# Kernel tuning notes

Measured on AMD Instinct MI355X. Metric: run time of the kernel, lower is better.

Reference implementation:

```python
import jax, jax.numpy as jnp
import numpy as np

D_MODEL = 1024
NUM_SLOTS = 4096
MIN_K = 8
MAX_K = 32


def setup_inputs() -> dict:
    key = jax.random.key(0)
    k1, k2, k3 = jax.random.split(key, 3)
    x = jax.random.normal(k1, (4, 1024, D_MODEL), dtype=jnp.float32)
    param_pool = 0.02 * jax.random.normal(k2, (NUM_SLOTS, D_MODEL), dtype=jnp.float32)
    w_router = 0.02 * jax.random.normal(k3, (D_MODEL, NUM_SLOTS), dtype=jnp.float32)
    return {"x": x, "param_pool": param_pool, "w_router": w_router}


def _route(x, w_router):
    # Router: linear projection to slot logits, softmax, dynamic top-k in [MIN_K, MAX_K].
    logits = jnp.einsum('bsd,dn->bsn', x, w_router)           # [B,S,N]
    probs = jax.nn.softmax(logits, axis=-1)
    top_probs, indices = jax.lax.top_k(probs, MAX_K)          # [B,S,K]
    # dynamic k: always keep first MIN_K slots; keep up to MAX_K while prob > uniform
    pos = jnp.arange(MAX_K)
    keep = (pos < MIN_K) | (top_probs > (1.0 / NUM_SLOTS))    # [B,S,K] bool
    keep_f = keep.astype(top_probs.dtype)
    masked = top_probs * keep_f
    weights = masked / (jnp.sum(masked, axis=-1, keepdims=True) + 1e-9)
    # load-balancing aux loss: N * sum(mean_prob_per_slot * frac_tokens_routed_per_slot)
    mean_probs = jnp.mean(probs, axis=(0, 1))                 # [N]
    counts = jnp.zeros((NUM_SLOTS,), dtype=jnp.float32).at[indices.reshape(-1)].add(keep_f.reshape(-1))
    frac = counts / (jnp.sum(keep_f) + 1e-9)
    aux_loss = NUM_SLOTS * jnp.sum(mean_probs * frac)
    return indices, weights, keep, aux_loss


def reference(x, param_pool, w_router):
    indices, weights, keep, aux_loss = _route(x, w_router)
    selected_params = param_pool[indices]                      # [B,S,K,D] gather
    proj = jnp.einsum('bsd,bskd->bsk', x, selected_params)     # per-token dot scores
    weighted_proj = proj * weights
    output = jnp.einsum('bsk,bskd->bsd', weighted_proj, selected_params)
    flat_indices = indices.reshape(-1)
    flat_keep = keep.reshape(-1)
    touched = jnp.zeros((NUM_SLOTS,), dtype=jnp.bool_).at[flat_indices].max(flat_keep)
    active_count = jnp.sum(touched)
    return (output, aux_loss, active_count)
```

## Files before the change

### kernel.cpp

```cpp
#include <hip/hip_runtime.h>
#include <math.h>
#include <stdint.h>

#define D_MODEL   1024
#define NUM_SLOTS 4096
#define N_TOKENS  4096
#define MIN_K     8
#define MAX_K     32
#define KP        1024
#define NSTEP     32

typedef _Float16 f16x8 __attribute__((ext_vector_type(8)));
typedef _Float16 f16x4 __attribute__((ext_vector_type(4)));
typedef float    f32x4 __attribute__((ext_vector_type(4)));

__device__ __forceinline__ void gload16(const void* g, void* l) {
    __builtin_amdgcn_global_load_lds((const __attribute__((address_space(1))) void*)g,
                                     (__attribute__((address_space(3))) void*)l,
                                     16, 0, 0);
}

__device__ __forceinline__ uint32_t bf16rn(float f) {
    uint32_t u = __float_as_uint(f);
    return (u + 0x7FFFu + ((u >> 16) & 1u)) >> 16;
}

__device__ __forceinline__ uint32_t ford(float f) {
    uint32_t b = __float_as_uint(f);
    return b ^ (uint32_t)(((int32_t)b >> 31) | 0x80000000);
}

__global__ __launch_bounds__(256) void pack_all(const float* __restrict__ x,
                                                const float* __restrict__ w,
                                                const float* __restrict__ pool,
                                                _Float16* __restrict__ A,
                                                _Float16* __restrict__ BT,
                                                uint32_t* __restrict__ poolbf,
                                                float* __restrict__ clr) {
    __shared__ float tile[64][65];
    const int bid = blockIdx.x;
    const int tid = threadIdx.x;

    if (bid < 4096) {
        if (bid < 32) clr[bid * 256 + tid] = 0.f;
        const int i = bid * 256 + tid;
        const float4 v = reinterpret_cast<const float4*>(x)[i];
        const int t = i >> 8;
        const int d = (i & 255) << 2;
        f16x4 hi;
        hi[0] = (_Float16)v.x; hi[1] = (_Float16)v.y;
        hi[2] = (_Float16)v.z; hi[3] = (_Float16)v.w;
        *(f16x4*)(A + (size_t)t * KP + d) = hi;
    } else if (bid < 5120) {
        const int b2 = bid - 4096;
        const int n0 = (b2 & 63) * 64;
        const int k0 = (b2 >> 6) * 64;
        {
            const int c  = tid & 63;
            const int r0 = tid >> 6;
#pragma unroll
            for (int i = 0; i < 16; ++i) {
                const int r = r0 * 16 + i;
                tile[r][c] = w[(size_t)(k0 + r) * NUM_SLOTS + n0 + c];
            }
        }
        __syncthreads();
        const int nl  = tid >> 2;
        const int kl0 = (tid & 3) * 16;
        _Float16* rowp = BT + (size_t)(n0 + nl) * KP + k0;
#pragma unroll
        for (int j4 = 0; j4 < 16; j4 += 4) {
            f16x4 hi;
#pragma unroll
            for (int u = 0; u < 4; ++u)
                hi[u] = (_Float16)tile[kl0 + j4 + u][nl];
            *(f16x4*)(rowp + kl0 + j4) = hi;
        }
    } else {
        const size_t i = (size_t)(bid - 5120) * 256 + tid;
        const float4* s4 = reinterpret_cast<const float4*>(pool);
        const float4 a = s4[2 * i];
        const float4 b = s4[2 * i + 1];
        uint4 u;
        u.x = bf16rn(a.x) | (bf16rn(a.y) << 16);
        u.y = bf16rn(a.z) | (bf16rn(a.w) << 16);
        u.z = bf16rn(b.x) | (bf16rn(b.y) << 16);
        u.w = bf16rn(b.z) | (bf16rn(b.w) << 16);
        reinterpret_cast<uint4*>(poolbf)[i] = u;
    }
}

#define STAGE_A(NXT, S2) \
    gload16(gA0 + (size_t)(S2) * 32, (void*)(AsF + (NXT) * 8192 + tid * 8)); \
    gload16(gA1 + (size_t)(S2) * 32, (void*)(AsF + (NXT) * 8192 + 4096 + tid * 8));
#define STAGE_B(NXT, S2) \
    gload16(gB0 + (size_t)(S2) * 32, (void*)(BsF + (NXT) * 8192 + tid * 8)); \
    gload16(gB1 + (size_t)(S2) * 32, (void*)(BsF + (NXT) * 8192 + 4096 + tid * 8));

#define MM(AF, M) \
    acc[M][0] = __builtin_amdgcn_mfma_f32_16x16x32_f16(AF, bf0, acc[M][0], 0, 0, 0); \
    acc[M][1] = __builtin_amdgcn_mfma_f32_16x16x32_f16(AF, bf1, acc[M][1], 0, 0, 0); \
    acc[M][2] = __builtin_amdgcn_mfma_f32_16x16x32_f16(AF, bf2, acc[M][2], 0, 0, 0); \
    acc[M][3] = __builtin_amdgcn_mfma_f32_16x16x32_f16(AF, bf3, acc[M][3], 0, 0, 0);

#define GSTEP(S, CUR, NXT) do { \
    const _Float16* a_ = AsF + (CUR) * 8192; \
    const _Float16* b_ = BsF + (CUR) * 8192; \
    f16x8 bf0 = *(const f16x8*)(b_ + offB0); \
    f16x8 bf1 = *(const f16x8*)(b_ + offB1); \
    f16x8 bf2 = *(const f16x8*)(b_ + offB2); \
    f16x8 bf3 = *(const f16x8*)(b_ + offB3); \
    f16x8 a0 = *(const f16x8*)(a_ + offA0); \
    f16x8 a1 = *(const f16x8*)(a_ + offA1); \
    f16x8 a2 = *(const f16x8*)(a_ + offA2); \
    f16x8 a3 = *(const f16x8*)(a_ + offA3); \
    if ((S) + 2 < NSTEP) { STAGE_A(NXT, (S) + 2) } \
    asm volatile("" ::: "memory"); \
    __builtin_amdgcn_s_barrier(); \
    __builtin_amdgcn_s_setprio(1); \
    MM(a0, 0) MM(a1, 1) MM(a2, 2) MM(a3, 3) \
    __builtin_amdgcn_s_setprio(0); \
    asm volatile("" ::: "memory"); \
    __builtin_amdgcn_s_barrier(); \
    a0 = *(const f16x8*)(a_ + offA4); \
    a1 = *(const f16x8*)(a_ + offA5); \
    a2 = *(const f16x8*)(a_ + offA6); \
    a3 = *(const f16x8*)(a_ + offA7); \
    if ((S) + 2 < NSTEP) { STAGE_B(NXT, (S) + 2) } \
    asm volatile("" ::: "memory"); \
    __builtin_amdgcn_s_barrier(); \
    __builtin_amdgcn_s_setprio(1); \
    MM(a0, 4) MM(a1, 5) MM(a2, 6) MM(a3, 7) \
    __builtin_amdgcn_s_setprio(0); \
    if ((S) < NSTEP - 2) { asm volatile("s_waitcnt vmcnt(4)" ::: "memory"); } \
    else                 { asm volatile("s_waitcnt vmcnt(0)" ::: "memory"); } \
    __builtin_amdgcn_s_barrier(); \
} while (0)

__global__ __launch_bounds__(512, 2) void gemm256(const _Float16* __restrict__ A,
                                                  const _Float16* __restrict__ BT,
                                                  float* __restrict__ C,
                                                  int nbm) {
    __shared__ _Float16 AsF[4 * 8192];
    __shared__ _Float16 BsF[4 * 8192];
    const int tid  = threadIdx.x;
    const int lane = tid & 63;
    const int wv   = tid >> 6;
    const int wm   = wv >> 2;
    const int wn   = wv & 3;

    int brow, bcol;
    {
        const int bid = blockIdx.x;
        if (nbm == 16) {
            const int xcd = bid & 7;
            const int l   = bid >> 3;
            brow = (xcd & 3) * 4 + (l & 3);
            bcol = (xcd >> 2) * 8 + (l >> 2);
        } else {
            brow = bid >> 4;
            bcol = bid & 15;
        }
    }
    const size_t bm = (size_t)brow * 256;
    const size_t bn = (size_t)bcol * 256;

    const int rowA = tid >> 2;
    const int slot = tid & 3;
    const int sswz = slot ^ ((rowA >> 1) & 3);
    const _Float16* gA0 = A  + (bm + rowA) * (size_t)KP + sswz * 8;
    const _Float16* gA1 = A  + (bm + rowA + 128) * (size_t)KP + sswz * 8;
    const _Float16* gB0 = BT + (bn + rowA) * (size_t)KP + sswz * 8;
    const _Float16* gB1 = BT + (bn + rowA + 128) * (size_t)KP + sswz * 8;

    int offA0, offA1, offA2, offA3, offA4, offA5, offA6, offA7;
    int offB0, offB1, offB2, offB3;
    {
        const int r15 = lane & 15, ls = lane >> 4;
#define AOFF(M) (((wm) * 128 + (M) * 16 + r15) * 32 + \
                 ((ls ^ ((((wm) * 128 + (M) * 16 + r15) >> 1) & 3)) * 8))
#define BOFF(N) (((wn) * 64 + (N) * 16 + r15) * 32 + \
                 ((ls ^ ((((wn) * 64 + (N) * 16 + r15) >> 1) & 3)) * 8))
        offA0 = AOFF(0); offA1 = AOFF(1); offA2 = AOFF(2); offA3 = AOFF(3);
        offA4 = AOFF(4); offA5 = AOFF(5); offA6 = AOFF(6); offA7 = AOFF(7);
        offB0 = BOFF(0); offB1 = BOFF(1); offB2 = BOFF(2); offB3 = BOFF(3);
#undef AOFF
#undef BOFF
    }

    f32x4 acc[8][4] = {};

    STAGE_A(0, 0) STAGE_B(0, 0)
    STAGE_A(1, 1) STAGE_B(1, 1)
    asm volatile("s_waitcnt vmcnt(4)" ::: "memory");
    __builtin_amdgcn_s_barrier();

    for (int s4 = 0; s4 < NSTEP; s4 += 4) {
        GSTEP(s4 + 0, 0, 2);
        GSTEP(s4 + 1, 1, 3);
        GSTEP(s4 + 2, 2, 0);
        GSTEP(s4 + 3, 3, 1);
    }

    const size_t crow = bm + wm * 128 + ((lane >> 4) << 2);
    const size_t ccol = bn + wn * 64 + (lane & 15);
#pragma unroll
    for (int m = 0; m < 8; ++m)
#pragma unroll
        for (int r = 0; r < 4; ++r) {
            float* cp = C + (crow + m * 16 + r) * (size_t)NUM_SLOTS + ccol;
#pragma unroll
            for (int n = 0; n < 4; ++n) cp[n * 16] = acc[m][n][r];
        }
}

#define RECOMP(G, A, B, Cc, D) do { \
    uint32_t t0 = (msk & (1u << (A)))  ? k##A  : 0u; \
    uint32_t t1 = (msk & (1u << (B)))  ? k##B  : 0u; \
    uint32_t t2 = (msk & (1u << (Cc))) ? k##Cc : 0u; \
    uint32_t t3 = (msk & (1u << (D)))  ? k##D  : 0u; \
    t0 = t0 > t1 ? t0 : t1; t2 = t2 > t3 ? t2 : t3; \
    gm##G = t0 > t2 ? t0 : t2; } while (0)

#define UNPK8(q, a0,a1,a2,a3,a4,a5,a6,a7) \
    a0 = __uint_as_float((q).x << 16); a1 = __uint_as_float((q).x & 0xFFFF0000u); \
    a2 = __uint_as_float((q).y << 16); a3 = __uint_as_float((q).y & 0xFFFF0000u); \
    a4 = __uint_as_float((q).z << 16); a5 = __uint_as_float((q).z & 0xFFFF0000u); \
    a6 = __uint_as_float((q).w << 16); a7 = __uint_as_float((q).w & 0xFFFF0000u);

__global__ __launch_bounds__(256) void router_kernel(
    const float* __restrict__ logits,
    const float* __restrict__ x,
    const uint32_t* __restrict__ poolbf,
    float* __restrict__ out,
    float2* __restrict__ minv,
    float* __restrict__ counts) {
    __shared__ float    s_union[NUM_SLOTS];
    __shared__ uint32_t s_cand[128];
    __shared__ float    s_redv[4];

    const int tid  = threadIdx.x;
    const int w    = tid >> 6;
    const int lane = tid & 63;
    const int wseg = w << 10;
    const int t    = blockIdx.x;

    const float4* lrow4 =
        reinterpret_cast<const float4*>(logits + (size_t)t * NUM_SLOTS + wseg);

    float4 lv0, lv1, lv2, lv3;
    lv0 = lrow4[lane];
    lv1 = lrow4[lane + 64];
    lv2 = lrow4[lane + 128];
    lv3 = lrow4[lane + 192];
    reinterpret_cast<float4*>(s_union + wseg)[lane]       = lv0;
    reinterpret_cast<float4*>(s_union + wseg)[lane + 64]  = lv1;
    reinterpret_cast<float4*>(s_union + wseg)[lane + 128] = lv2;
    reinterpret_cast<float4*>(s_union + wseg)[lane + 192] = lv3;
    float lmax = fmaxf(fmaxf(fmaxf(lv0.x, lv0.y), fmaxf(lv0.z, lv0.w)),
                       fmaxf(fmaxf(lv1.x, lv1.y), fmaxf(lv1.z, lv1.w)));
    lmax = fmaxf(lmax, fmaxf(fmaxf(lv2.x, lv2.y), fmaxf(lv2.z, lv2.w)));
    lmax = fmaxf(lmax, fmaxf(fmaxf(lv3.x, lv3.y), fmaxf(lv3.z, lv3.w)));
#pragma unroll
    for (int o = 32; o; o >>= 1) lmax = fmaxf(lmax, __shfl_xor(lmax, o));
    if (lane == 0) s_redv[w] = lmax;
    __syncthreads();
    const float m = fmaxf(fmaxf(s_redv[0], s_redv[1]), fmaxf(s_redv[2], s_redv[3]));
    __syncthreads();

    float lsum;
    {
        float4 ev0, ev1, ev2, ev3;
        ev0.x = __expf(lv0.x - m); ev0.y = __expf(lv0.y - m);
        ev0.z = __expf(lv0.z - m); ev0.w = __expf(lv0.w - m);
        ev1.x = __expf(lv1.x - m); ev1.y = __expf(lv1.y - m);
        ev1.z = __expf(lv1.z - m); ev1.w = __expf(lv1.w - m);
        ev2.x = __expf(lv2.x - m); ev2.y = __expf(lv2.y - m);
        ev2.z = __expf(lv2.z - m); ev2.w = __expf(lv2.w - m);
        ev3.x = __expf(lv3.x - m); ev3.y = __expf(lv3.y - m);
        ev3.z = __expf(lv3.z - m); ev3.w = __expf(lv3.w - m);
        lsum = (ev0.x + ev0.y + ev0.z + ev0.w) + (ev1.x + ev1.y + ev1.z + ev1.w) +
               (ev2.x + ev2.y + ev2.z + ev2.w) + (ev3.x + ev3.y + ev3.z + ev3.w);
    }
#pragma unroll
    for (int o = 32; o; o >>= 1) lsum += __shfl_xor(lsum, o);
    if (lane == 0) s_redv[w] = lsum;
    __syncthreads();
    const float inv = 1.0f / (s_redv[0] + s_redv[1] + s_redv[2] + s_redv[3]);
    if (tid == 0) minv[t] = make_float2(m, inv);

    const int kb = wseg + 4 * lane;
    uint32_t k0  = (ford(lv0.x) & 0xFFFFF000u) | (uint32_t)(4095 - (kb + 0));
    uint32_t k1  = (ford(lv0.y) & 0xFFFFF000u) | (uint32_t)(4095 - (kb + 1));
    uint32_t k2  = (ford(lv0.z) & 0xFFFFF000u) | (uint32_t)(4095 - (kb + 2));
    uint32_t k3  = (ford(lv0.w) & 0xFFFFF000u) | (uint32_t)(4095 - (kb + 3));
    uint32_t k4  = (ford(lv1.x) & 0xFFFFF000u) | (uint32_t)(4095 - (kb + 256));
    uint32_t k5  = (ford(lv1.y) & 0xFFFFF000u) | (uint32_t)(4095 - (kb + 257));
    uint32_t k6  = (ford(lv1.z) & 0xFFFFF000u) | (uint32_t)(4095 - (kb + 258));
    uint32_t k7  = (ford(lv1.w) & 0xFFFFF000u) | (uint32_t)(4095 - (kb + 259));
    uint32_t k8  = (ford(lv2.x) & 0xFFFFF000u) | (uint32_t)(4095 - (kb + 512));
    uint32_t k9  = (ford(lv2.y) & 0xFFFFF000u) | (uint32_t)(4095 - (kb + 513));
    uint32_t k10 = (ford(lv2.z) & 0xFFFFF000u) | (uint32_t)(4095 - (kb + 514));
    uint32_t k11 = (ford(lv2.w) & 0xFFFFF000u) | (uint32_t)(4095 - (kb + 515));
    uint32_t k12 = (ford(lv3.x) & 0xFFFFF000u) | (uint32_t)(4095 - (kb + 768));
    uint32_t k13 = (ford(lv3.y) & 0xFFFFF000u) | (uint32_t)(4095 - (kb + 769));
    uint32_t k14 = (ford(lv3.z) & 0xFFFFF000u) | (uint32_t)(4095 - (kb + 770));
    uint32_t k15 = (ford(lv3.w) & 0xFFFFF000u) | (uint32_t)(4095 - (kb + 771));

    uint32_t msk = 0xFFFFu;
    uint32_t gm0, gm1, gm2, gm3;
    RECOMP(0, 0, 1, 2, 3); RECOMP(1, 4, 5, 6, 7);
    RECOMP(2, 8, 9, 10, 11); RECOMP(3, 12, 13, 14, 15);

    uint32_t kept = 0;
    for (int it = 0; it < 32; ++it) {
        uint32_t best = gm0;
        if (gm1 > best) best = gm1;
        if (gm2 > best) best = gm2;
        if (gm3 > best) best = gm3;
        uint32_t wb = best;
#pragma unroll
        for (int o = 32; o; o >>= 1) {
            const uint32_t p = __shfl_xor(wb, o);
            if (p > wb) wb = p;
        }
        if (lane == it) kept = wb;
        if (best == wb) {
            const int idx = 4095 - (int)(wb & 0xFFFu);
            const int rem = idx - kb;
            const int jj = rem >> 8;
            msk &= ~(1u << (4 * jj + (rem & 3)));
            switch (jj) {
                case 0:  RECOMP(0, 0, 1, 2, 3); break;
                case 1:  RECOMP(1, 4, 5, 6, 7); break;
                case 2:  RECOMP(2, 8, 9, 10, 11); break;
                default: RECOMP(3, 12, 13, 14, 15); break;
            }
        }
    }
    if (lane < 32) s_cand[w * 32 + lane] = kept;
    __syncthreads();

    uint32_t v0 = s_cand[lane];
    uint32_t v1 = s_cand[64 + lane];
#pragma unroll
    for (int k = 2; k <= 128; k <<= 1) {
#pragma unroll
        for (int j = k >> 1; j > 0; j >>= 1) {
            if (j == 64) {
                const uint32_t a = v0 > v1 ? v0 : v1;
                const uint32_t b = v0 > v1 ? v1 : v0;
                v0 = a; v1 = b;
            } else {
                const bool jl = (lane & j) == 0;
                {
                    const uint32_t p = __shfl_xor(v0, j);
                    const bool km = ((lane & k) == 0) == jl;
                    v0 = ((p > v0) == km) ? p : v0;
                }
                {
                    const uint32_t p = __shfl_xor(v1, j);
                    const bool km = (((lane + 64) & k) == 0) == jl;
                    v1 = ((p > v1) == km) ? p : v1;
                }
            }
        }
    }

    const int slotv = 4095 - (int)(v0 & 0xFFFu);
    float pv = 0.f;
    if (lane < 32) pv = __expf(s_union[slotv] - m) * inv;
    const bool kp = (lane < MIN_K) || (pv > (1.0f / 4096.0f));
    float wsum = kp ? pv : 0.f;
#pragma unroll
    for (int o = 32; o; o >>= 1) wsum += __shfl_xor(wsum, o);
    const float wgtl = kp ? pv / (wsum + 1e-9f) : 0.f;
    if (w == 0 && lane < 32 && kp) atomicAdd(&counts[slotv], 1.0f);
    __syncthreads();

    const float4* x4 = reinterpret_cast<const float4*>(x + (size_t)t * D_MODEL);
    const float4 xa0 = x4[2 * lane];
    const float4 xb0 = x4[2 * lane + 1];
    const float4 xa1 = x4[2 * lane + 128];
    const float4 xb1 = x4[2 * lane + 129];
    float4 oa0 = {0,0,0,0}, ob0 = {0,0,0,0}, oa1 = {0,0,0,0}, ob1 = {0,0,0,0};

#pragma unroll
    for (int ii = 0; ii < 8; ++ii) {
        const int   i     = w * 8 + ii;
        const int   slotg = __shfl(slotv, i);
        const float wgt   = __shfl(wgtl, i);
        if (wgt != 0.f) {
            const uint4* pr = reinterpret_cast<const uint4*>(poolbf + (size_t)slotg * (D_MODEL / 2));
            const uint4 q0 = pr[lane];
            const uint4 q1 = pr[lane + 64];
            float pA0,pA1,pA2,pA3,pA4,pA5,pA6,pA7;
            float pB0,pB1,pB2,pB3,pB4,pB5,pB6,pB7;
            UNPK8(q0, pA0,pA1,pA2,pA3,pA4,pA5,pA6,pA7)
            UNPK8(q1, pB0,pB1,pB2,pB3,pB4,pB5,pB6,pB7)
            float d;
            d = xa0.x * pA0;
            d = fmaf(xa0.y, pA1, d); d = fmaf(xa0.z, pA2, d); d = fmaf(xa0.w, pA3, d);
            d = fmaf(xb0.x, pA4, d); d = fmaf(xb0.y, pA5, d); d = fmaf(xb0.z, pA6, d); d = fmaf(xb0.w, pA7, d);
            d = fmaf(xa1.x, pB0, d); d = fmaf(xa1.y, pB1, d); d = fmaf(xa1.z, pB2, d); d = fmaf(xa1.w, pB3, d);
            d = fmaf(xb1.x, pB4, d); d = fmaf(xb1.y, pB5, d); d = fmaf(xb1.z, pB6, d); d = fmaf(xb1.w, pB7, d);
#pragma unroll
            for (int o = 32; o; o >>= 1) d += __shfl_xor(d, o);
            const float wp = d * wgt;
            oa0.x = fmaf(wp, pA0, oa0.x); oa0.y = fmaf(wp, pA1, oa0.y);
            oa0.z = fmaf(wp, pA2, oa0.z); oa0.w = fmaf(wp, pA3, oa0.w);
            ob0.x = fmaf(wp, pA4, ob0.x); ob0.y = fmaf(wp, pA5, ob0.y);
            ob0.z = fmaf(wp, pA6, ob0.z); ob0.w = fmaf(wp, pA7, ob0.w);
            oa1.x = fmaf(wp, pB0, oa1.x); oa1.y = fmaf(wp, pB1, oa1.y);
            oa1.z = fmaf(wp, pB2, oa1.z); oa1.w = fmaf(wp, pB3, oa1.w);
            ob1.x = fmaf(wp, pB4, ob1.x); ob1.y = fmaf(wp, pB5, ob1.y);
            ob1.z = fmaf(wp, pB6, ob1.z); ob1.w = fmaf(wp, pB7, ob1.w);
        }
    }

    {
        float4* op = reinterpret_cast<float4*>(s_union + w * 1024);
        op[2 * lane]       = oa0;
        op[2 * lane + 1]   = ob0;
        op[2 * lane + 128] = oa1;
        op[2 * lane + 129] = ob1;
    }
    __syncthreads();
    float4 r = {0, 0, 0, 0};
#pragma unroll
    for (int ww = 0; ww < 4; ++ww) {
        const float4 vv = reinterpret_cast<const float4*>(s_union + ww * 1024)[tid];
        r.x += vv.x; r.y += vv.y; r.z += vv.z; r.w += vv.w;
    }
    reinterpret_cast<float4*>(out + (size_t)t * D_MODEL)[tid] = r;
}

__global__ __launch_bounds__(256) void colsum_lg(const float* __restrict__ logits,
                                                 const float2* __restrict__ minv,
                                                 float* __restrict__ colsum) {
    const int tid = threadIdx.x;
    const int s0  = blockIdx.x * 1024;
    const int t0  = blockIdx.y * 64;
    float a0 = 0.f, a1 = 0.f, a2 = 0.f, a3 = 0.f;
    for (int t = 0; t < 64; ++t) {
        const float2 mv = minv[t0 + t];
        const float4 v = reinterpret_cast<const float4*>(
            logits + (size_t)(t0 + t) * NUM_SLOTS + s0)[tid];
        a0 = fmaf(__expf(v.x - mv.x), mv.y, a0);
        a1 = fmaf(__expf(v.y - mv.x), mv.y, a1);
        a2 = fmaf(__expf(v.z - mv.x), mv.y, a2);
        a3 = fmaf(__expf(v.w - mv.x), mv.y, a3);
    }
    const int c = s0 + 4 * tid;
    atomicAdd(&colsum[c + 0], a0);
    atomicAdd(&colsum[c + 1], a1);
    atomicAdd(&colsum[c + 2], a2);
    atomicAdd(&colsum[c + 3], a3);
}

__global__ __launch_bounds__(256) void finalize_kernel(
    const float* __restrict__ counts,
    const float* __restrict__ colsum,
    float* __restrict__ out2) {
    __shared__ float s_tot[4], s_act[4], s_dot[4];
    const int tid = threadIdx.x;
    float tot = 0.f, act = 0.f, dot = 0.f;
#pragma unroll
    for (int j = 0; j < 16; ++j) {
        const int i = j * 256 + tid;
        const float c = counts[i];
        tot += c;
        act += (c > 0.f) ? 1.f : 0.f;
        dot += colsum[i] * c;
    }
#pragma unroll
    for (int o = 32; o; o >>= 1) {
        tot += __shfl_xor(tot, o);
        act += __shfl_xor(act, o);
        dot += __shfl_xor(dot, o);
    }
    if ((tid & 63) == 0) {
        s_tot[tid >> 6] = tot; s_act[tid >> 6] = act; s_dot[tid >> 6] = dot;
    }
    __syncthreads();
    if (tid == 0) {
        const float T  = s_tot[0] + s_tot[1] + s_tot[2] + s_tot[3];
        const float A  = s_act[0] + s_act[1] + s_act[2] + s_act[3];
        const float Dt = s_dot[0] + s_dot[1] + s_dot[2] + s_dot[3];
        out2[0] = Dt / (T + 1e-9f);
        out2[1] = A;
    }
}

extern "C" void kernel_launch(void* const* d_in, const int* in_sizes, int n_in,
                              void* d_out, int out_size, void* d_ws, size_t ws_size,
                              hipStream_t stream) {
    const float* x    = (const float*)d_in[0];
    const float* pool = (const float*)d_in[1];
    const float* w    = (const float*)d_in[2];
    float* out = (float*)d_out;

    const size_t MB = 1024 * 1024;
    char* ws = (char*)d_ws;
    float*     colsum = (float*)ws;
    float*     counts = (float*)(ws + 16 * 1024);
    float2*    minv   = (float2*)(ws + 32 * 1024);
    uint32_t*  poolbf = (uint32_t*)(ws + 64 * 1024);
    _Float16*  Apack  = (_Float16*)(ws + 64 * 1024 + 8 * MB);
    _Float16*  Bpack  = (_Float16*)(ws + 64 * 1024 + 16 * MB);
    float*     logits = (float*)(ws + 64 * 1024 + 24 * MB);

    pack_all<<<7168, 256, 0, stream>>>(x, w, pool, Apack, Bpack, poolbf, colsum);

    gemm256<<<16 * 16, 512, 0, stream>>>(Apack, Bpack, logits, 16);

    router_kernel<<<N_TOKENS, 256, 0, stream>>>(logits, x, poolbf, out,
                                                minv, counts);

    colsum_lg<<<dim3(NUM_SLOTS / 1024, N_TOKENS / 64), 256, 0, stream>>>(
        logits, minv, colsum);

    finalize_kernel<<<1, 256, 0, stream>>>(counts, colsum, out + (out_size - 2));
}
```

Baseline: 146.8 us.

## Speculative 16-per-wave top-k with fallback to full 32-per-wave selection

Each wave now extracts only its top 16 candidates instead of 32, then publishes its 17th-best value. A 64-wide bitonic sort merges the candidates. If the global 32nd-best beats every wave's 17th-best, the result is exact. Otherwise the kernel reloads the keys from shared memory and reruns the original 32-round selection and 128-wide sort. The weighted gather loop also drops its wgt!=0 branch so it runs unconditionally, which keeps the control flow uniform but loads pool rows for dropped slots.

After: 198.8 us. 35.4% more time.

```diff
diff --git a/kernel.cpp b/kernel.cpp
--- a/kernel.cpp
+++ b/kernel.cpp
@@ -222,6 +222,32 @@
     t0 = t0 > t1 ? t0 : t1; t2 = t2 > t3 ? t2 : t3; \
     gm##G = t0 > t2 ? t0 : t2; } while (0)
 
+#define XROUND(IT) do { \
+    uint32_t best = gm0; \
+    if (gm1 > best) best = gm1; \
+    if (gm2 > best) best = gm2; \
+    if (gm3 > best) best = gm3; \
+    uint32_t wb = best; \
+    _Pragma("unroll") \
+    for (int o = 32; o; o >>= 1) { \
+        const uint32_t p = __shfl_xor(wb, o); \
+        if (p > wb) wb = p; \
+    } \
+    if (lane == (IT)) kept = wb; \
+    if (best == wb) { \
+        const int idx = 4095 - (int)(wb & 0xFFFu); \
+        const int rem = idx - kb; \
+        const int jj = rem >> 8; \
+        msk &= ~(1u << (4 * jj + (rem & 3))); \
+        switch (jj) { \
+            case 0:  RECOMP(0, 0, 1, 2, 3); break; \
+            case 1:  RECOMP(1, 4, 5, 6, 7); break; \
+            case 2:  RECOMP(2, 8, 9, 10, 11); break; \
+            default: RECOMP(3, 12, 13, 14, 15); break; \
+        } \
+    } \
+} while (0)
+
 #define UNPK8(q, a0,a1,a2,a3,a4,a5,a6,a7) \
     a0 = __uint_as_float((q).x << 16); a1 = __uint_as_float((q).x & 0xFFFF0000u); \
     a2 = __uint_as_float((q).y << 16); a3 = __uint_as_float((q).y & 0xFFFF0000u); \
@@ -313,55 +339,92 @@
     RECOMP(2, 8, 9, 10, 11); RECOMP(3, 12, 13, 14, 15);
 
     uint32_t kept = 0;
-    for (int it = 0; it < 32; ++it) {
+    for (int it = 0; it < 16; ++it) { XROUND(it); }
+
+    {
         uint32_t best = gm0;
         if (gm1 > best) best = gm1;
         if (gm2 > best) best = gm2;
         if (gm3 > best) best = gm3;
-        uint32_t wb = best;
 #pragma unroll
         for (int o = 32; o; o >>= 1) {
-            const uint32_t p = __shfl_xor(wb, o);
-            if (p > wb) wb = p;
-        }
-        if (lane == it) kept = wb;
-        if (best == wb) {
-            const int idx = 4095 - (int)(wb & 0xFFFu);
-            const int rem = idx - kb;
-            const int jj = rem >> 8;
-            msk &= ~(1u << (4 * jj + (rem & 3)));
-            switch (jj) {
-                case 0:  RECOMP(0, 0, 1, 2, 3); break;
-                case 1:  RECOMP(1, 4, 5, 6, 7); break;
-                case 2:  RECOMP(2, 8, 9, 10, 11); break;
-                default: RECOMP(3, 12, 13, 14, 15); break;
-            }
-        }
-    }
-    if (lane < 32) s_cand[w * 32 + lane] = kept;
+            const uint32_t p = __shfl_xor(best, o);
+            if (p > best) best = p;
+        }
+        if (lane == 0) s_cand[64 + w] = best;
+    }
+    if (lane < 16) s_cand[w * 16 + lane] = kept;
     __syncthreads();
 
     uint32_t v0 = s_cand[lane];
-    uint32_t v1 = s_cand[64 + lane];
-#pragma unroll
-    for (int k = 2; k <= 128; k <<= 1) {
+#pragma unroll
+    for (int k = 2; k <= 64; k <<= 1) {
 #pragma unroll
         for (int j = k >> 1; j > 0; j >>= 1) {
-            if (j == 64) {
-                const uint32_t a = v0 > v1 ? v0 : v1;
-                const uint32_t b = v0 > v1 ? v1 : v0;
-                v0 = a; v1 = b;
-            } else {
-                const bool jl = (lane & j) == 0;
-                {
-                    const uint32_t p = __shfl_xor(v0, j);
-                    const bool km = ((lane & k) == 0) == jl;
-                    v0 = ((p > v0) == km) ? p : v0;
-                }
-                {
-                    const uint32_t p = __shfl_xor(v1, j);
-                    const bool km = (((lane + 64) & k) == 0) == jl;
-                    v1 = ((p > v1) == km) ? p : v1;
+            const bool jl = (lane & j) == 0;
+            const uint32_t p = __shfl_xor(v0, j);
+            const bool km = ((lane & k) == 0) == jl;
+            v0 = ((p > v0) == km) ? p : v0;
+        }
+    }
+
+    const uint32_t th = __shfl(v0, 31);
+    uint32_t mw = s_cand[64];
+    {
+        const uint32_t m1 = s_cand[65], m2 = s_cand[66], m3 = s_cand[67];
+        if (m1 > mw) mw = m1;
+        if (m2 > mw) mw = m2;
+        if (m3 > mw) mw = m3;
+    }
+    if (th < mw) {
+        __syncthreads();
+        const float* lw = s_union + wseg;
+        const int lb = 4 * lane;
+        k0  = (ford(lw[lb + 0])   & 0xFFFFF000u) | (uint32_t)(4095 - (kb + 0));
+        k1  = (ford(lw[lb + 1])   & 0xFFFFF000u) | (uint32_t)(4095 - (kb + 1));
+        k2  = (ford(lw[lb + 2])   & 0xFFFFF000u) | (uint32_t)(4095 - (kb + 2));
+        k3  = (ford(lw[lb + 3])   & 0xFFFFF000u) | (uint32_t)(4095 - (kb + 3));
+        k4  = (ford(lw[lb + 256]) & 0xFFFFF000u) | (uint32_t)(4095 - (kb + 256));
+        k5  = (ford(lw[lb + 257]) & 0xFFFFF000u) | (uint32_t)(4095 - (kb + 257));
+        k6  = (ford(lw[lb + 258]) & 0xFFFFF000u) | (uint32_t)(4095 - (kb + 258));
+        k7  = (ford(lw[lb + 259]) & 0xFFFFF000u) | (uint32_t)(4095 - (kb + 259));
+        k8  = (ford(lw[lb + 512]) & 0xFFFFF000u) | (uint32_t)(4095 - (kb + 512));
+        k9  = (ford(lw[lb + 513]) & 0xFFFFF000u) | (uint32_t)(4095 - (kb + 513));
+        k10 = (ford(lw[lb + 514]) & 0xFFFFF000u) | (uint32_t)(4095 - (kb + 514));
+        k11 = (ford(lw[lb + 515]) & 0xFFFFF000u) | (uint32_t)(4095 - (kb + 515));
+        k12 = (ford(lw[lb + 768]) & 0xFFFFF000u) | (uint32_t)(4095 - (kb + 768));
+        k13 = (ford(lw[lb + 769]) & 0xFFFFF000u) | (uint32_t)(4095 - (kb + 769));
+        k14 = (ford(lw[lb + 770]) & 0xFFFFF000u) | (uint32_t)(4095 - (kb + 770));
+        k15 = (ford(lw[lb + 771]) & 0xFFFFF000u) | (uint32_t)(4095 - (kb + 771));
+        msk = 0xFFFFu;
+        RECOMP(0, 0, 1, 2, 3); RECOMP(1, 4, 5, 6, 7);
+        RECOMP(2, 8, 9, 10, 11); RECOMP(3, 12, 13, 14, 15);
+        for (int it = 0; it < 32; ++it) { XROUND(it); }
+        if (lane < 32) s_cand[w * 32 + lane] = kept;
+        __syncthreads();
+
+        v0 = s_cand[lane];
+        uint32_t v1 = s_cand[64 + lane];
+#pragma unroll
+        for (int k = 2; k <= 128; k <<= 1) {
+#pragma unroll
+            for (int j = k >> 1; j > 0; j >>= 1) {
+                if (j == 64) {
+                    const uint32_t a = v0 > v1 ? v0 : v1;
+                    const uint32_t b = v0 > v1 ? v1 : v0;
+                    v0 = a; v1 = b;
+                } else {
+                    const bool jl = (lane & j) == 0;
+                    {
+                        const uint32_t p = __shfl_xor(v0, j);
+                        const bool km = ((lane & k) == 0) == jl;
+                        v0 = ((p > v0) == km) ? p : v0;
+                    }
+                    {
+                        const uint32_t p = __shfl_xor(v1, j);
+                        const bool km = (((lane + 64) & k) == 0) == jl;
+                        v1 = ((p > v1) == km) ? p : v1;
+                    }
                 }
             }
         }
@@ -390,32 +453,30 @@
         const int   i     = w * 8 + ii;
         const int   slotg = __shfl(slotv, i);
         const float wgt   = __shfl(wgtl, i);
-        if (wgt != 0.f) {
-            const uint4* pr = reinterpret_cast<const uint4*>(poolbf + (size_t)slotg * (D_MODEL / 2));
-            const uint4 q0 = pr[lane];
-            const uint4 q1 = pr[lane + 64];
-            float pA0,pA1,pA2,pA3,pA4,pA5,pA6,pA7;
-            float pB0,pB1,pB2,pB3,pB4,pB5,pB6,pB7;
-            UNPK8(q0, pA0,pA1,pA2,pA3,pA4,pA5,pA6,pA7)
-            UNPK8(q1, pB0,pB1,pB2,pB3,pB4,pB5,pB6,pB7)
-            float d;
-            d = xa0.x * pA0;
-            d = fmaf(xa0.y, pA1, d); d = fmaf(xa0.z, pA2, d); d = fmaf(xa0.w, pA3, d);
-            d = fmaf(xb0.x, pA4, d); d = fmaf(xb0.y, pA5, d); d = fmaf(xb0.z, pA6, d); d = fmaf(xb0.w, pA7, d);
-            d = fmaf(xa1.x, pB0, d); d = fmaf(xa1.y, pB1, d); d = fmaf(xa1.z, pB2, d); d = fmaf(xa1.w, pB3, d);
-            d = fmaf(xb1.x, pB4, d); d = fmaf(xb1.y, pB5, d); d = fmaf(xb1.z, pB6, d); d = fmaf(xb1.w, pB7, d);
-#pragma unroll
-            for (int o = 32; o; o >>= 1) d += __shfl_xor(d, o);
-            const float wp = d * wgt;
-            oa0.x = fmaf(wp, pA0, oa0.x); oa0.y = fmaf(wp, pA1, oa0.y);
-            oa0.z = fmaf(wp, pA2, oa0.z); oa0.w = fmaf(wp, pA3, oa0.w);
-            ob0.x = fmaf(wp, pA4, ob0.x); ob0.y = fmaf(wp, pA5, ob0.y);
-            ob0.z = fmaf(wp, pA6, ob0.z); ob0.w = fmaf(wp, pA7, ob0.w);
-            oa1.x = fmaf(wp, pB0, oa1.x); oa1.y = fmaf(wp, pB1, oa1.y);
-            oa1.z = fmaf(wp, pB2, oa1.z); oa1.w = fmaf(wp, pB3, oa1.w);
-            ob1.x = fmaf(wp, pB4, ob1.x); ob1.y = fmaf(wp, pB5, ob1.y);
-            ob1.z = fmaf(wp, pB6, ob1.z); ob1.w = fmaf(wp, pB7, ob1.w);
-        }
+        const uint4* pr = reinterpret_cast<const uint4*>(poolbf + (size_t)slotg * (D_MODEL / 2));
+        const uint4 q0 = pr[lane];
+        const uint4 q1 = pr[lane + 64];
+        float pA0,pA1,pA2,pA3,pA4,pA5,pA6,pA7;
+        float pB0,pB1,pB2,pB3,pB4,pB5,pB6,pB7;
+        UNPK8(q0, pA0,pA1,pA2,pA3,pA4,pA5,pA6,pA7)
+        UNPK8(q1, pB0,pB1,pB2,pB3,pB4,pB5,pB6,pB7)
+        float d;
+        d = xa0.x * pA0;
+        d = fmaf(xa0.y, pA1, d); d = fmaf(xa0.z, pA2, d); d = fmaf(xa0.w, pA3, d);
+        d = fmaf(xb0.x, pA4, d); d = fmaf(xb0.y, pA5, d); d = fmaf(xb0.z, pA6, d); d = fmaf(xb0.w, pA7, d);
+        d = fmaf(xa1.x, pB0, d); d = fmaf(xa1.y, pB1, d); d = fmaf(xa1.z, pB2, d); d = fmaf(xa1.w, pB3, d);
+        d = fmaf(xb1.x, pB4, d); d = fmaf(xb1.y, pB5, d); d = fmaf(xb1.z, pB6, d); d = fmaf(xb1.w, pB7, d);
+#pragma unroll
+        for (int o = 32; o; o >>= 1) d += __shfl_xor(d, o);
+        const float wp = d * wgt;
+        oa0.x = fmaf(wp, pA0, oa0.x); oa0.y = fmaf(wp, pA1, oa0.y);
+        oa0.z = fmaf(wp, pA2, oa0.z); oa0.w = fmaf(wp, pA3, oa0.w);
+        ob0.x = fmaf(wp, pA4, ob0.x); ob0.y = fmaf(wp, pA5, ob0.y);
+        ob0.z = fmaf(wp, pA6, ob0.z); ob0.w = fmaf(wp, pA7, ob0.w);
+        oa1.x = fmaf(wp, pB0, oa1.x); oa1.y = fmaf(wp, pB1, oa1.y);
+        oa1.z = fmaf(wp, pB2, oa1.z); oa1.w = fmaf(wp, pB3, oa1.w);
+        ob1.x = fmaf(wp, pB4, ob1.x); ob1.y = fmaf(wp, pB5, ob1.y);
+        ob1.z = fmaf(wp, pB6, ob1.z); ob1.w = fmaf(wp, pB7, ob1.w);
     }
 
     {
```
